# Performance work log

Measured on AMD Instinct MI355X. Metric: run time of the kernel, lower is better.

Reference implementation:

```python
import jax, jax.numpy as jnp
import numpy as np

N_NODES = 50000
N_EDGES = 650000
NEG_SLOPE = 0.2


def gat_conv(x, src, dst, W, a_src, a_dst, bias, concat):
    """PyG-style GATConv (eval mode, self-loops already included in src/dst).
    x: [N, F_in], W: [F_in, H*C], a_src/a_dst: [H, C], bias: [H*C] or [C]."""
    N = x.shape[0]
    H, C = a_src.shape
    h = (x @ W).reshape(N, H, C)                      # [N, H, C]
    al_src = (h * a_src).sum(-1)                      # [N, H]
    al_dst = (h * a_dst).sum(-1)                      # [N, H]
    logits = jax.nn.leaky_relu(al_src[src] + al_dst[dst], NEG_SLOPE)  # [E, H]
    # segment softmax over destination neighborhoods
    m = jax.ops.segment_max(logits, dst, num_segments=N)
    m = jnp.where(jnp.isfinite(m), m, 0.0)
    e = jnp.exp(logits - m[dst])
    s = jax.ops.segment_sum(e, dst, num_segments=N)
    alpha = e / (s[dst] + 1e-16)                      # [E, H]
    msg = alpha[:, :, None] * h[src]                  # [E, H, C]
    out = jax.ops.segment_sum(msg, dst, num_segments=N)  # [N, H, C]
    out = out.reshape(N, H * C) if concat else out.mean(axis=1)
    return out + bias


def setup_inputs() -> dict:
    key = jax.random.key(0)
    ks = jax.random.split(key, 16)
    IN, HID, H, OUT = 128, 64, 4, 1
    x = jax.random.normal(ks[0], (N_NODES, IN), dtype=jnp.float32)
    edge_index = jax.random.randint(ks[1], (2, N_EDGES), 0, N_NODES, dtype=jnp.int64)
    s = 0.1
    params = {
        'W1': jax.random.normal(ks[2], (IN, H * HID), dtype=jnp.float32) * s,
        'a_src1': jax.random.normal(ks[3], (H, HID), dtype=jnp.float32) * s,
        'a_dst1': jax.random.normal(ks[4], (H, HID), dtype=jnp.float32) * s,
        'b1': jnp.zeros((H * HID,), dtype=jnp.float32),
        'W2': jax.random.normal(ks[5], (H * HID, H * HID), dtype=jnp.float32) * s,
        'a_src2': jax.random.normal(ks[6], (H, HID), dtype=jnp.float32) * s,
        'a_dst2': jax.random.normal(ks[7], (H, HID), dtype=jnp.float32) * s,
        'b2': jnp.zeros((H * HID,), dtype=jnp.float32),
        'W3': jax.random.normal(ks[8], (H * HID, OUT), dtype=jnp.float32) * s,
        'a_src3': jax.random.normal(ks[9], (1, OUT), dtype=jnp.float32) * s,
        'a_dst3': jax.random.normal(ks[10], (1, OUT), dtype=jnp.float32) * s,
        'b3': jnp.zeros((OUT,), dtype=jnp.float32),
    }
    return {'x': x, 'edge_index': edge_index, **params}


def reference(x, edge_index, W1, a_src1, a_dst1, b1, W2, a_src2, a_dst2, b2, W3, a_src3, a_dst3, b3):
    N = x.shape[0]
    loops = jnp.arange(N, dtype=edge_index.dtype)
    src = jnp.concatenate([edge_index[0], loops])
    dst = jnp.concatenate([edge_index[1], loops])
    h = gat_conv(x, src, dst, W1, a_src1, a_dst1, b1, concat=True)
    h = jax.nn.elu(h)  # dropout: identity in eval mode
    h = gat_conv(h, src, dst, W2, a_src2, a_dst2, b2, concat=True)
    h = jax.nn.elu(h)
    out = gat_conv(h, src, dst, W3, a_src3, a_dst3, b3, concat=False)
    return out
```

## Files before the change

kernel.cpp:

```cpp
#include <hip/hip_runtime.h>
#include <math.h>

#define NN 50000
#define NE 650000
#define NET 700000
#define FD 256
#define NEG 0.2f
#define NB 49

static __device__ __forceinline__ float lrelu(float v){ return v > 0.f ? v : NEG*v; }

static __device__ __forceinline__ unsigned short f2bf(float f){
  union { float f; unsigned u; } v; v.f = f;
  unsigned r = v.u + 0x7fff + ((v.u >> 16) & 1);
  return (unsigned short)(r >> 16);
}
static __device__ __forceinline__ float bf2f(unsigned short h){
  union { unsigned u; float f; } v; v.u = ((unsigned)h) << 16;
  return v.f;
}
static __device__ __forceinline__ float bflo(unsigned u){ return __uint_as_float(u << 16); }
static __device__ __forceinline__ float bfhi(unsigned u){ return __uint_as_float(u & 0xffff0000u); }

static __device__ __forceinline__ void gload_lds16(const unsigned short* g, unsigned short* l){
  __builtin_amdgcn_global_load_lds(
      (const __attribute__((address_space(1))) unsigned int*)(g),
      (__attribute__((address_space(3))) unsigned int*)(l), 16, 0, 0);
}

typedef __attribute__((ext_vector_type(8))) short short8_t;
typedef __attribute__((ext_vector_type(4))) float f32x4;

#define NX (NN*128)
#define CAST_ELEMS (NX + 128*256 + 256*256)
#define CAST_BLOCKS ((CAST_ELEMS/4 + 255)/256)
#define CNT_BLOCKS ((NET + 255)/256)
__global__ void init_fused(const float* __restrict__ x, const float* __restrict__ W1,
                           const float* __restrict__ W2,
                           unsigned short* __restrict__ xh, unsigned short* __restrict__ xl,
                           unsigned short* __restrict__ bt1h, unsigned short* __restrict__ bt1l,
                           unsigned short* __restrict__ bt2h, unsigned short* __restrict__ bt2l,
                           const int* __restrict__ ei, int* __restrict__ deg){
  int b = blockIdx.x;
  if (b >= CAST_BLOCKS){
    int e = (b - CAST_BLOCKS)*256 + threadIdx.x;
    if (e < NET){
      int d = (e < NE) ? ei[NE + e] : (e - NE);
      atomicAdd(&deg[d], 1);
    }
    return;
  }
  int i = (b*256 + threadIdx.x)*4;
  if (i < NX){
    float4 f = *(const float4*)(x + i);
    ushort4 h, l;
    h.x = f2bf(f.x); l.x = f2bf(f.x - bf2f(h.x));
    h.y = f2bf(f.y); l.y = f2bf(f.y - bf2f(h.y));
    h.z = f2bf(f.z); l.z = f2bf(f.z - bf2f(h.z));
    h.w = f2bf(f.w); l.w = f2bf(f.w - bf2f(h.w));
    *(ushort4*)(xh + i) = h;
    *(ushort4*)(xl + i) = l;
    return;
  }
  int e, K;
  const float* B;
  unsigned short *bh, *bl;
  if (i < NX + 128*256){ e = i - NX; K = 128; B = W1; bh = bt1h; bl = bt1l; }
  else if (i < CAST_ELEMS){ e = i - NX - 128*256; K = 256; B = W2; bh = bt2h; bl = bt2l; }
  else return;
  int k = e >> 8, n = e & 255;
  float4 f = *(const float4*)(B + e);
  #pragma unroll
  for (int j=0;j<4;j++){
    float fv = (j==0)?f.x:(j==1)?f.y:(j==2)?f.z:f.w;
    unsigned short h = f2bf(fv);
    bh[(n+j)*K + k] = h;
    bl[(n+j)*K + k] = f2bf(fv - bf2f(h));
  }
}

__global__ void scan_block(const int* __restrict__ deg, int* __restrict__ excl, int* __restrict__ bsums){
  __shared__ int sh[256];
  int t = threadIdx.x;
  int i0 = blockIdx.x*1024 + t*4;
  int v0 = (i0+0 < NN) ? deg[i0+0] : 0;
  int v1 = (i0+1 < NN) ? deg[i0+1] : 0;
  int v2 = (i0+2 < NN) ? deg[i0+2] : 0;
  int v3 = (i0+3 < NN) ? deg[i0+3] : 0;
  int tot = v0+v1+v2+v3;
  sh[t] = tot;
  __syncthreads();
  for (int off=1; off<256; off<<=1){
    int x = (t>=off) ? sh[t-off] : 0;
    __syncthreads();
    sh[t] += x;
    __syncthreads();
  }
  int base = sh[t] - tot;
  if (i0+0 < NN) excl[i0+0] = base;
  if (i0+1 < NN) excl[i0+1] = base + v0;
  if (i0+2 < NN) excl[i0+2] = base + v0+v1;
  if (i0+3 < NN) excl[i0+3] = base + v0+v1+v2;
  if (t == 255) bsums[blockIdx.x] = sh[255];
}

__global__ void scan_add(int* __restrict__ indptr, const int* __restrict__ bsums, int* __restrict__ cursor){
  __shared__ int boff[64];
  if (threadIdx.x < 64){
    int lane = threadIdx.x;
    int v = (lane < NB) ? bsums[lane] : 0;
    int orig = v;
    for (int off=1; off<64; off<<=1){
      int u = __shfl_up(v, off);
      if (lane >= off) v += u;
    }
    boff[lane] = v - orig;
  }
  __syncthreads();
  int i = blockIdx.x*blockDim.x + threadIdx.x;
  if (i < NN){
    int v = indptr[i] + boff[i>>10];
    indptr[i] = v;
    cursor[i] = v;
  }
  if (i == 0) indptr[NN] = NET;
}

__global__ void scatter_csr(const int* __restrict__ ei, int* __restrict__ cursor, int* __restrict__ csr){
  int e = blockIdx.x*blockDim.x + threadIdx.x;
  if (e >= NET) return;
  int s, d;
  if (e < NE){ s = ei[e]; d = ei[NE+e]; } else { s = e-NE; d = e-NE; }
  int pos = atomicAdd(&cursor[d], 1);
  csr[pos] = s;
}

template<int K>
__global__ __launch_bounds__(256, 3) void gemm_mfma(const unsigned short* __restrict__ Ahg,
                                                    const unsigned short* __restrict__ Alg,
                                                    const unsigned short* __restrict__ Bth,
                                                    const unsigned short* __restrict__ Btl,
                                                    unsigned short* __restrict__ Cb,
                                                    const float* __restrict__ a_src,
                                                    const float* __restrict__ a_dst,
                                                    float* __restrict__ al,
                                                    int M){
  constexpr int ITERS = K/32;
  __shared__ unsigned short Ah[128*32], Al[128*32], Bh[128*32], Bl[128*32];
  int t = threadIdx.x;
  int wave = t >> 6, lane = t & 63;
  int wm = wave >> 1, wn = wave & 1;
  int quad = lane >> 4, l16 = lane & 15;
  int bm0 = blockIdx.y*128, bn0 = blockIdx.x*128;

  const unsigned short* gsrc = (wave==0)?Ahg:(wave==1)?Alg:(wave==2)?Bth:Btl;
  unsigned short* lbuf       = (wave==0)?Ah :(wave==1)?Al :(wave==2)?Bh :Bl;
  int sbase = (wave < 2) ? bm0 : bn0;
  int srow = lane >> 2;
  int skg  = (lane & 3) * 8;

  const unsigned short* gp[8];
  #pragma unroll
  for (int i=0;i<8;i++){
    int r = sbase + i*16 + srow;
    if (wave < 2) r = min(r, M-1);
    gp[i] = gsrc + (size_t)r*K + skg;
  }

  f32x4 acc[4][4];
  #pragma unroll
  for (int i=0;i<4;i++)
    #pragma unroll
    for (int j=0;j<4;j++) acc[i][j] = (f32x4){0.f,0.f,0.f,0.f};

  #pragma unroll
  for (int i=0;i<8;i++) gload_lds16(gp[i], lbuf + i*512);

  #pragma unroll
  for (int it=0; it<ITERS; ++it){
    __syncthreads();

    short8_t afh[4], afl[4], bfh[4], bfl[4];
    #pragma unroll
    for (int mt=0; mt<4; ++mt){
      int row = wm*64 + mt*16 + l16;
      afh[mt] = *(short8_t*)&Ah[row*32 + quad*8];
      afl[mt] = *(short8_t*)&Al[row*32 + quad*8];
    }
    #pragma unroll
    for (int nt=0; nt<4; ++nt){
      int col = wn*64 + nt*16 + l16;
      bfh[nt] = *(short8_t*)&Bh[col*32 + quad*8];
      bfl[nt] = *(short8_t*)&Bl[col*32 + quad*8];
    }
    __syncthreads();

    if (it+1 < ITERS){
      int k0 = (it+1)*32;
      #pragma unroll
      for (int i=0;i<8;i++) gload_lds16(gp[i] + k0, lbuf + i*512);
    }

    #pragma unroll
    for (int mt=0; mt<4; ++mt)
      #pragma unroll
      for (int nt=0; nt<4; ++nt){
        acc[mt][nt] = __builtin_amdgcn_mfma_f32_16x16x32_bf16(afh[mt], bfh[nt], acc[mt][nt], 0,0,0);
        acc[mt][nt] = __builtin_amdgcn_mfma_f32_16x16x32_bf16(afh[mt], bfl[nt], acc[mt][nt], 0,0,0);
        acc[mt][nt] = __builtin_amdgcn_mfma_f32_16x16x32_bf16(afl[mt], bfh[nt], acc[mt][nt], 0,0,0);
      }
  }

  int head_w = (bn0 >> 6) + wn;
  float cs[4], cd[4];
  #pragma unroll
  for (int nt=0; nt<4; ++nt){
    cs[nt] = a_src[head_w*64 + nt*16 + l16];
    cd[nt] = a_dst[head_w*64 + nt*16 + l16];
  }
  {
    float* fsc = (float*)lbuf;
    int grow = bm0 + wm*64 + lane;
    #pragma unroll
    for (int pass=0; pass<2; ++pass){
      #pragma unroll
      for (int mt=0; mt<4; ++mt)
        #pragma unroll
        for (int r=0; r<4; ++r){
          float p = 0.f;
          #pragma unroll
          for (int nt=0; nt<4; ++nt)
            p += acc[mt][nt][r] * (pass ? cd[nt] : cs[nt]);
          fsc[(mt*16 + quad*4 + r)*17 + l16] = p;
        }
      float s = 0.f;
      #pragma unroll
      for (int j=0; j<16; ++j) s += fsc[lane*17 + j];
      if (grow < M) al[grow*8 + pass*4 + head_w] = s;
    }
  }

  unsigned short* tile = lbuf;
  #pragma unroll
  for (int mt=0; mt<4; ++mt)
    #pragma unroll
    for (int r=0; r<4; ++r){
      int rl = mt*16 + quad*4 + r;
      #pragma unroll
      for (int nt=0; nt<4; ++nt)
        tile[rl*64 + nt*16 + l16] = f2bf(acc[mt][nt][r]);
    }
  int orow = lane >> 3, ocol = (lane & 7) * 8;
  #pragma unroll
  for (int it=0; it<8; ++it){
    int rl = it*8 + orow;
    int row = bm0 + wm*64 + rl;
    if (row < M){
      uint4 v = *(uint4*)&tile[rl*64 + ocol];
      *(uint4*)(Cb + (size_t)row*FD + bn0 + wn*64 + ocol) = v;
    }
  }
}

template<bool FUSE_W3>
__global__ __launch_bounds__(256) void gat_agg(const unsigned short* __restrict__ hb,
                                               const float* __restrict__ al,
                                               const int* __restrict__ indptr, const int* __restrict__ csr,
                                               const float* __restrict__ bias,
                                               unsigned short* __restrict__ outh,
                                               unsigned short* __restrict__ outl,
                                               const float* __restrict__ W3,
                                               float* __restrict__ h3){
  __shared__ float ebuf[8][128];
  __shared__ int   sbuf[8][32];
  int wave = threadIdx.x >> 6, lane = threadIdx.x & 63;
  int half = lane >> 5, l32 = lane & 31;
  int slot = wave*2 + half;
  int n = blockIdx.x*8 + slot;
  if (n >= NN) return;
  int head8 = l32 >> 3;
  int2 ip = *(const int2*)(indptr + n);
  int base = ip.x, deg = ip.y - ip.x;
  float4 ald = *(const float4*)(al + n*8 + 4);
  float* eb = &ebuf[slot][0];
  int*   sb = &sbuf[slot][0];
  const char* hp = (const char*)hb + l32*16;

  float acc[8] = {0.f,0.f,0.f,0.f,0.f,0.f,0.f,0.f};
  float4 esum = make_float4(0.f,0.f,0.f,0.f);

  for (int j0 = 0; j0 < deg; j0 += 32){
    int j = j0 + l32;
    float4 e4 = make_float4(0.f,0.f,0.f,0.f);
    int sj = 0;
    if (j < deg){
      sj = csr[base + j];
      float4 als = *(const float4*)(al + sj*8);
      e4.x = __expf(lrelu(als.x + ald.x));
      e4.y = __expf(lrelu(als.y + ald.y));
      e4.z = __expf(lrelu(als.z + ald.z));
      e4.w = __expf(lrelu(als.w + ald.w));
      esum.x += e4.x; esum.y += e4.y; esum.z += e4.z; esum.w += e4.w;
    }
    *(float4*)&eb[l32*4] = e4;
    sb[l32] = sj << 9;
    int cnt  = min(32, deg - j0);
    int cpad = (cnt + 7) & ~7;
    for (int tt = 0; tt < cpad; tt += 8){
      uint4 r[8];
      float v[8];
      #pragma unroll
      for (int q=0; q<8; ++q){
        int o = sb[tt+q];
        v[q] = eb[(tt+q)*4 + head8];
        r[q] = *(const uint4*)(hp + o);
      }
      #pragma unroll
      for (int q=0; q<8; ++q){
        acc[0]+=v[q]*bflo(r[q].x); acc[1]+=v[q]*bfhi(r[q].x);
        acc[2]+=v[q]*bflo(r[q].y); acc[3]+=v[q]*bfhi(r[q].y);
        acc[4]+=v[q]*bflo(r[q].z); acc[5]+=v[q]*bfhi(r[q].z);
        acc[6]+=v[q]*bflo(r[q].w); acc[7]+=v[q]*bfhi(r[q].w);
      }
    }
  }

  for (int off=16; off; off>>=1){
    esum.x += __shfl_xor(esum.x, off);
    esum.y += __shfl_xor(esum.y, off);
    esum.z += __shfl_xor(esum.z, off);
    esum.w += __shfl_xor(esum.w, off);
  }
  float sH = (head8==0)?esum.x:(head8==1)?esum.y:(head8==2)?esum.z:esum.w;
  float inv = 1.f/(sH + 1e-16f);
  int ch0 = l32*8;
  float4 b0 = *(const float4*)(bias + ch0);
  float4 b1 = *(const float4*)(bias + ch0 + 4);
  float o[8];
  o[0]=acc[0]*inv+b0.x; o[1]=acc[1]*inv+b0.y; o[2]=acc[2]*inv+b0.z; o[3]=acc[3]*inv+b0.w;
  o[4]=acc[4]*inv+b1.x; o[5]=acc[5]*inv+b1.y; o[6]=acc[6]*inv+b1.z; o[7]=acc[7]*inv+b1.w;
  #pragma unroll
  for (int i=0;i<8;i++) o[i] = o[i] > 0.f ? o[i] : expm1f(o[i]);

  if (FUSE_W3){
    float4 w0 = *(const float4*)(W3 + ch0);
    float4 w1 = *(const float4*)(W3 + ch0 + 4);
    float p = o[0]*w0.x + o[1]*w0.y + o[2]*w0.z + o[3]*w0.w
            + o[4]*w1.x + o[5]*w1.y + o[6]*w1.z + o[7]*w1.w;
    #pragma unroll
    for (int off=16; off; off>>=1) p += __shfl_xor(p, off);
    if (l32 == 0) h3[n] = p;
  } else {
    unsigned hi[4], lo[4];
    #pragma unroll
    for (int i=0;i<4;i++){
      unsigned short h0 = f2bf(o[2*i]),   h1 = f2bf(o[2*i+1]);
      unsigned short g0 = f2bf(o[2*i]   - bf2f(h0));
      unsigned short g1 = f2bf(o[2*i+1] - bf2f(h1));
      hi[i] = (unsigned)h0 | ((unsigned)h1 << 16);
      lo[i] = (unsigned)g0 | ((unsigned)g1 << 16);
    }
    *(uint4*)(outh + (size_t)n*FD + ch0) = make_uint4(hi[0],hi[1],hi[2],hi[3]);
    *(uint4*)(outl + (size_t)n*FD + ch0) = make_uint4(lo[0],lo[1],lo[2],lo[3]);
  }
}

__global__ __launch_bounds__(256) void gat_agg3(const float* __restrict__ h3, const int* __restrict__ indptr,
                                                const int* __restrict__ csr, const float* __restrict__ asrc,
                                                const float* __restrict__ adst, const float* __restrict__ b3,
                                                float* __restrict__ out){
  int tid = blockIdx.x*blockDim.x + threadIdx.x;
  int n = tid >> 2, sub = tid & 3;
  if (n >= NN) return;
  float as = asrc[0], ad = adst[0];
  float hd = h3[n]*ad;
  int2 ip = *(const int2*)(indptr + n);
  float s = 0.f, w = 0.f;
  for (int e = ip.x + sub; e < ip.y; e += 4){
    float hv = h3[csr[e]];
    float ee = __expf(lrelu(as*hv + hd));
    s += ee; w += ee*hv;
  }
  s += __shfl_xor(s, 1); w += __shfl_xor(w, 1);
  s += __shfl_xor(s, 2); w += __shfl_xor(w, 2);
  if (sub == 0) out[n] = w/(s + 1e-16f) + b3[0];
}

extern "C" void kernel_launch(void* const* d_in, const int* in_sizes, int n_in,
                              void* d_out, int out_size, void* d_ws, size_t ws_size,
                              hipStream_t stream){
  const float* x   = (const float*)d_in[0];
  const int*   ei  = (const int*)d_in[1];
  const float* W1  = (const float*)d_in[2];
  const float* as1 = (const float*)d_in[3];
  const float* ad1 = (const float*)d_in[4];
  const float* b1  = (const float*)d_in[5];
  const float* W2  = (const float*)d_in[6];
  const float* as2 = (const float*)d_in[7];
  const float* ad2 = (const float*)d_in[8];
  const float* b2  = (const float*)d_in[9];
  const float* W3  = (const float*)d_in[10];
  const float* as3 = (const float*)d_in[11];
  const float* ad3 = (const float*)d_in[12];
  const float* b3  = (const float*)d_in[13];
  float* outp = (float*)d_out;

  char* w = (char*)d_ws;
  size_t off = 0;
  auto alloc = [&](size_t bytes)->void*{
    void* p = w + off; off += (bytes + 255) & ~(size_t)255; return p;
  };
  unsigned short* hb  = (unsigned short*)alloc((size_t)NN*FD*2);
  unsigned short* oh  = (unsigned short*)alloc((size_t)NN*FD*2);
  unsigned short* ol  = (unsigned short*)alloc((size_t)NN*FD*2);
  unsigned short* xh  = (unsigned short*)alloc((size_t)NN*128*2);
  unsigned short* xl  = (unsigned short*)alloc((size_t)NN*128*2);
  float* al    = (float*)alloc((size_t)NN*8*4);
  int*   indptr= (int*)alloc((size_t)(NN+1)*4);
  int*   cursor= (int*)alloc((size_t)NN*4);
  int*   csr   = (int*)alloc((size_t)NET*4);
  int*   bsums = (int*)alloc(64*4);
  float* h3    = (float*)alloc((size_t)NN*4);
  unsigned short* bt1h = (unsigned short*)alloc((size_t)256*128*2);
  unsigned short* bt1l = (unsigned short*)alloc((size_t)256*128*2);
  unsigned short* bt2h = (unsigned short*)alloc((size_t)256*256*2);
  unsigned short* bt2l = (unsigned short*)alloc((size_t)256*256*2);

  hipMemsetAsync(cursor, 0, (size_t)NN*4, stream);
  init_fused<<<CAST_BLOCKS + CNT_BLOCKS, 256, 0, stream>>>(x, W1, W2, xh, xl,
                                                           bt1h, bt1l, bt2h, bt2l,
                                                           ei, cursor);
  scan_block<<<NB, 256, 0, stream>>>(cursor, indptr, bsums);
  scan_add<<<(NN+255)/256, 256, 0, stream>>>(indptr, bsums, cursor);
  scatter_csr<<<(NET+255)/256, 256, 0, stream>>>(ei, cursor, csr);

  dim3 gemm_grid(FD/128, (NN+127)/128);
  int agg_blocks = (NN+7)/8;

  gemm_mfma<128><<<gemm_grid, 256, 0, stream>>>(xh, xl, bt1h, bt1l, hb, as1, ad1, al, NN);
  gat_agg<false><<<agg_blocks, 256, 0, stream>>>(hb, al, indptr, csr, b1, oh, ol, nullptr, nullptr);
  gemm_mfma<256><<<gemm_grid, 256, 0, stream>>>(oh, ol, bt2h, bt2l, hb, as2, ad2, al, NN);
  gat_agg<true><<<agg_blocks, 256, 0, stream>>>(hb, al, indptr, csr, b2, nullptr, nullptr, W3, h3);
  gat_agg3<<<(NN*4+255)/256, 256, 0, stream>>>(h3, indptr, csr, as3, ad3, b3, outp);
}
```

Baseline: 343.9 us.

## Use 2-wave 64x128 GEMM warp tiles and single-block degree scan

The GEMM now runs with 128 threads per block. Each of the two waves computes a 64x128 output tile with 32 accumulators, so B fragments are reused across more MFMAs and fewer waves share the LDS staging. The two-kernel prefix scan is replaced by one single-block 1024-thread scan that carries totals across chunks, which removes a launch and the block-sums buffer. The cost is heavier register pressure (128 accumulator floats per lane), fewer waves to hide latency, and a serial scan that runs on a single CU.

```diff
diff --git a/kernel.cpp b/kernel.cpp
--- a/kernel.cpp
+++ b/kernel.cpp
@@ -6,7 +6,6 @@
 #define NET 700000
 #define FD 256
 #define NEG 0.2f
-#define NB 49
 
 static __device__ __forceinline__ float lrelu(float v){ return v > 0.f ? v : NEG*v; }
 
@@ -79,51 +78,40 @@
   }
 }
 
-__global__ void scan_block(const int* __restrict__ deg, int* __restrict__ excl, int* __restrict__ bsums){
-  __shared__ int sh[256];
-  int t = threadIdx.x;
-  int i0 = blockIdx.x*1024 + t*4;
-  int v0 = (i0+0 < NN) ? deg[i0+0] : 0;
-  int v1 = (i0+1 < NN) ? deg[i0+1] : 0;
-  int v2 = (i0+2 < NN) ? deg[i0+2] : 0;
-  int v3 = (i0+3 < NN) ? deg[i0+3] : 0;
-  int tot = v0+v1+v2+v3;
-  sh[t] = tot;
+__global__ __launch_bounds__(1024) void scan_all(const int* __restrict__ deg,
+                                                 int* __restrict__ indptr,
+                                                 int* __restrict__ cursor){
+  __shared__ int wsum[16];
+  __shared__ int carrysh;
+  int t = threadIdx.x, w = t >> 6, lane = t & 63;
+  if (t == 0) carrysh = 0;
   __syncthreads();
-  for (int off=1; off<256; off<<=1){
-    int x = (t>=off) ? sh[t-off] : 0;
+  for (int c = 0; c < (NN + 1023)/1024; ++c){
+    int i = c*1024 + t;
+    int v = (i < NN) ? deg[i] : 0;
+    int s = v;
+    for (int off=1; off<64; off<<=1){
+      int u = __shfl_up(s, off);
+      if (lane >= off) s += u;
+    }
+    if (lane == 63) wsum[w] = s;
     __syncthreads();
-    sh[t] += x;
+    if (t < 16){
+      int xx = wsum[t];
+      int e2 = xx;
+      for (int off=1; off<16; off<<=1){
+        int u = __shfl_up(e2, off);
+        if (t >= off) e2 += u;
+      }
+      wsum[t] = e2 - xx;
+    }
     __syncthreads();
-  }
-  int base = sh[t] - tot;
-  if (i0+0 < NN) excl[i0+0] = base;
-  if (i0+1 < NN) excl[i0+1] = base + v0;
-  if (i0+2 < NN) excl[i0+2] = base + v0+v1;
-  if (i0+3 < NN) excl[i0+3] = base + v0+v1+v2;
-  if (t == 255) bsums[blockIdx.x] = sh[255];
-}
-
-__global__ void scan_add(int* __restrict__ indptr, const int* __restrict__ bsums, int* __restrict__ cursor){
-  __shared__ int boff[64];
-  if (threadIdx.x < 64){
-    int lane = threadIdx.x;
-    int v = (lane < NB) ? bsums[lane] : 0;
-    int orig = v;
-    for (int off=1; off<64; off<<=1){
-      int u = __shfl_up(v, off);
-      if (lane >= off) v += u;
-    }
-    boff[lane] = v - orig;
-  }
-  __syncthreads();
-  int i = blockIdx.x*blockDim.x + threadIdx.x;
-  if (i < NN){
-    int v = indptr[i] + boff[i>>10];
-    indptr[i] = v;
-    cursor[i] = v;
-  }
-  if (i == 0) indptr[NN] = NET;
+    int excl = s - v + wsum[w] + carrysh;
+    if (i < NN){ indptr[i] = excl; cursor[i] = excl; }
+    __syncthreads();
+    if (t == 1023) carrysh = excl + v;
+  }
+  if (t == 0) indptr[NN] = NET;
 }
 
 __global__ void scatter_csr(const int* __restrict__ ei, int* __restrict__ cursor, int* __restrict__ csr){
@@ -136,7 +124,7 @@
 }
 
 template<int K>
-__global__ __launch_bounds__(256, 3) void gemm_mfma(const unsigned short* __restrict__ Ahg,
+__global__ __launch_bounds__(128, 2) void gemm_mfma(const unsigned short* __restrict__ Ahg,
                                                     const unsigned short* __restrict__ Alg,
                                                     const unsigned short* __restrict__ Bth,
                                                     const unsigned short* __restrict__ Btl,
@@ -146,81 +134,92 @@
                                                     float* __restrict__ al,
                                                     int M){
   constexpr int ITERS = K/32;
-  __shared__ unsigned short Ah[128*32], Al[128*32], Bh[128*32], Bl[128*32];
+  __shared__ unsigned short smem[4*128*32];
+  unsigned short* Ah = smem;
+  unsigned short* Al = smem + 4096;
+  unsigned short* Bh = smem + 8192;
+  unsigned short* Bl = smem + 12288;
   int t = threadIdx.x;
   int wave = t >> 6, lane = t & 63;
-  int wm = wave >> 1, wn = wave & 1;
   int quad = lane >> 4, l16 = lane & 15;
   int bm0 = blockIdx.y*128, bn0 = blockIdx.x*128;
 
-  const unsigned short* gsrc = (wave==0)?Ahg:(wave==1)?Alg:(wave==2)?Bth:Btl;
-  unsigned short* lbuf       = (wave==0)?Ah :(wave==1)?Al :(wave==2)?Bh :Bl;
-  int sbase = (wave < 2) ? bm0 : bn0;
+  const unsigned short* g0 = wave ? Bth : Ahg;
+  const unsigned short* g1 = wave ? Btl : Alg;
+  unsigned short* l0 = wave ? Bh : Ah;
+  unsigned short* l1 = wave ? Bl : Al;
+  int sbase = wave ? bn0 : bm0;
   int srow = lane >> 2;
   int skg  = (lane & 3) * 8;
-
-  const unsigned short* gp[8];
+  int rr[8];
   #pragma unroll
   for (int i=0;i<8;i++){
     int r = sbase + i*16 + srow;
-    if (wave < 2) r = min(r, M-1);
-    gp[i] = gsrc + (size_t)r*K + skg;
-  }
-
-  f32x4 acc[4][4];
+    if (!wave) r = min(r, M-1);
+    rr[i] = r;
+  }
+  const unsigned short* g0p = g0 + skg;
+  const unsigned short* g1p = g1 + skg;
+
+  f32x4 acc[4][8];
   #pragma unroll
   for (int i=0;i<4;i++)
     #pragma unroll
-    for (int j=0;j<4;j++) acc[i][j] = (f32x4){0.f,0.f,0.f,0.f};
-
-  #pragma unroll
-  for (int i=0;i<8;i++) gload_lds16(gp[i], lbuf + i*512);
+    for (int j=0;j<8;j++) acc[i][j] = (f32x4){0.f,0.f,0.f,0.f};
+
+  #pragma unroll
+  for (int i=0;i<8;i++){
+    gload_lds16(g0p + (size_t)rr[i]*K, l0 + i*512);
+    gload_lds16(g1p + (size_t)rr[i]*K, l1 + i*512);
+  }
 
   #pragma unroll
   for (int it=0; it<ITERS; ++it){
     __syncthreads();
 
-    short8_t afh[4], afl[4], bfh[4], bfl[4];
-    #pragma unroll
-    for (int mt=0; mt<4; ++mt){
-      int row = wm*64 + mt*16 + l16;
-      afh[mt] = *(short8_t*)&Ah[row*32 + quad*8];
-      afl[mt] = *(short8_t*)&Al[row*32 + quad*8];
-    }
-    #pragma unroll
-    for (int nt=0; nt<4; ++nt){
-      int col = wn*64 + nt*16 + l16;
+    short8_t bfh[8], bfl[8];
+    #pragma unroll
+    for (int nt=0; nt<8; ++nt){
+      int col = nt*16 + l16;
       bfh[nt] = *(short8_t*)&Bh[col*32 + quad*8];
       bfl[nt] = *(short8_t*)&Bl[col*32 + quad*8];
     }
+    #pragma unroll
+    for (int mt=0; mt<4; ++mt){
+      int row = wave*64 + mt*16 + l16;
+      short8_t ah = *(short8_t*)&Ah[row*32 + quad*8];
+      short8_t alw = *(short8_t*)&Al[row*32 + quad*8];
+      #pragma unroll
+      for (int nt=0; nt<8; ++nt){
+        acc[mt][nt] = __builtin_amdgcn_mfma_f32_16x16x32_bf16(ah,  bfh[nt], acc[mt][nt], 0,0,0);
+        acc[mt][nt] = __builtin_amdgcn_mfma_f32_16x16x32_bf16(ah,  bfl[nt], acc[mt][nt], 0,0,0);
+        acc[mt][nt] = __builtin_amdgcn_mfma_f32_16x16x32_bf16(alw, bfh[nt], acc[mt][nt], 0,0,0);
+      }
+    }
     __syncthreads();
 
     if (it+1 < ITERS){
       int k0 = (it+1)*32;
       #pragma unroll
-      for (int i=0;i<8;i++) gload_lds16(gp[i] + k0, lbuf + i*512);
-    }
-
-    #pragma unroll
-    for (int mt=0; mt<4; ++mt)
-      #pragma unroll
-      for (int nt=0; nt<4; ++nt){
-        acc[mt][nt] = __builtin_amdgcn_mfma_f32_16x16x32_bf16(afh[mt], bfh[nt], acc[mt][nt], 0,0,0);
-        acc[mt][nt] = __builtin_amdgcn_mfma_f32_16x16x32_bf16(afh[mt], bfl[nt], acc[mt][nt], 0,0,0);
-        acc[mt][nt] = __builtin_amdgcn_mfma_f32_16x16x32_bf16(afl[mt], bfh[nt], acc[mt][nt], 0,0,0);
+      for (int i=0;i<8;i++){
+        gload_lds16(g0p + (size_t)rr[i]*K + k0, l0 + i*512);
+        gload_lds16(g1p + (size_t)rr[i]*K + k0, l1 + i*512);
       }
-  }
-
-  int head_w = (bn0 >> 6) + wn;
-  float cs[4], cd[4];
-  #pragma unroll
-  for (int nt=0; nt<4; ++nt){
-    cs[nt] = a_src[head_w*64 + nt*16 + l16];
-    cd[nt] = a_dst[head_w*64 + nt*16 + l16];
-  }
-  {
-    float* fsc = (float*)lbuf;
-    int grow = bm0 + wm*64 + lane;
+    }
+  }
+  unsigned short* scratch = smem + wave*8192;
+
+  int grow = bm0 + wave*64 + lane;
+  #pragma unroll
+  for (int h=0; h<2; ++h){
+    int head_w = (bn0 >> 6) + h;
+    float cs[4], cd[4];
+    #pragma unroll
+    for (int n4=0; n4<4; ++n4){
+      cs[n4] = a_src[head_w*64 + n4*16 + l16];
+      cd[n4] = a_dst[head_w*64 + n4*16 + l16];
+    }
+    float* fsc = (float*)scratch;
     #pragma unroll
     for (int pass=0; pass<2; ++pass){
       #pragma unroll
@@ -229,8 +228,8 @@
         for (int r=0; r<4; ++r){
           float p = 0.f;
           #pragma unroll
-          for (int nt=0; nt<4; ++nt)
-            p += acc[mt][nt][r] * (pass ? cd[nt] : cs[nt]);
+          for (int n4=0; n4<4; ++n4)
+            p += acc[mt][h*4+n4][r] * (pass ? cd[n4] : cs[n4]);
           fsc[(mt*16 + quad*4 + r)*17 + l16] = p;
         }
       float s = 0.f;
@@ -240,24 +239,24 @@
     }
   }
 
-  unsigned short* tile = lbuf;
+  unsigned short* tile = scratch;
   #pragma unroll
   for (int mt=0; mt<4; ++mt)
     #pragma unroll
     for (int r=0; r<4; ++r){
       int rl = mt*16 + quad*4 + r;
       #pragma unroll
-      for (int nt=0; nt<4; ++nt)
-        tile[rl*64 + nt*16 + l16] = f2bf(acc[mt][nt][r]);
-    }
-  int orow = lane >> 3, ocol = (lane & 7) * 8;
-  #pragma unroll
-  for (int it=0; it<8; ++it){
-    int rl = it*8 + orow;
-    int row = bm0 + wm*64 + rl;
+      for (int nt=0; nt<8; ++nt)
+        tile[rl*128 + nt*16 + l16] = f2bf(acc[mt][nt][r]);
+    }
+  int orow = lane >> 4, ocol = (lane & 15) * 8;
+  #pragma unroll
+  for (int it2=0; it2<16; ++it2){
+    int rl = it2*4 + orow;
+    int row = bm0 + wave*64 + rl;
     if (row < M){
-      uint4 v = *(uint4*)&tile[rl*64 + ocol];
-      *(uint4*)(Cb + (size_t)row*FD + bn0 + wn*64 + ocol) = v;
+      uint4 v = *(uint4*)&tile[rl*128 + ocol];
+      *(uint4*)(Cb + (size_t)row*FD + bn0 + ocol) = v;
     }
   }
 }
@@ -419,7 +418,6 @@
   int*   indptr= (int*)alloc((size_t)(NN+1)*4);
   int*   cursor= (int*)alloc((size_t)NN*4);
   int*   csr   = (int*)alloc((size_t)NET*4);
-  int*   bsums = (int*)alloc(64*4);
   float* h3    = (float*)alloc((size_t)NN*4);
   unsigned short* bt1h = (unsigned short*)alloc((size_t)256*128*2);
   unsigned short* bt1l = (unsigned short*)alloc((size_t)256*128*2);
@@ -430,16 +428,15 @@
   init_fused<<<CAST_BLOCKS + CNT_BLOCKS, 256, 0, stream>>>(x, W1, W2, xh, xl,
                                                            bt1h, bt1l, bt2h, bt2l,
                                                            ei, cursor);
-  scan_block<<<NB, 256, 0, stream>>>(cursor, indptr, bsums);
-  scan_add<<<(NN+255)/256, 256, 0, stream>>>(indptr, bsums, cursor);
+  scan_all<<<1, 1024, 0, stream>>>(cursor, indptr, cursor);
   scatter_csr<<<(NET+255)/256, 256, 0, stream>>>(ei, cursor, csr);
 
   dim3 gemm_grid(FD/128, (NN+127)/128);
   int agg_blocks = (NN+7)/8;
 
-  gemm_mfma<128><<<gemm_grid, 256, 0, stream>>>(xh, xl, bt1h, bt1l, hb, as1, ad1, al, NN);
+  gemm_mfma<128><<<gemm_grid, 128, 0, stream>>>(xh, xl, bt1h, bt1l, hb, as1, ad1, al, NN);
   gat_agg<false><<<agg_blocks, 256, 0, stream>>>(hb, al, indptr, csr, b1, oh, ol, nullptr, nullptr);
-  gemm_mfma<256><<<gemm_grid, 256, 0, stream>>>(oh, ol, bt2h, bt2l, hb, as2, ad2, al, NN);
+  gemm_mfma<256><<<gemm_grid, 128, 0, stream>>>(oh, ol, bt2h, bt2l, hb, as2, ad2, al, NN);
   gat_agg<true><<<agg_blocks, 256, 0, stream>>>(hb, al, indptr, csr, b2, nullptr, nullptr, W3, h3);
   gat_agg3<<<(NN*4+255)/256, 256, 0, stream>>>(h3, indptr, csr, as3, ad3, b3, outp);
 }
```

Result: slower. 388.4 us (+12.9%).
